# Performance work log

Hardware: AMD Instinct MI355X
Metric: run time of the kernel (lower is better)

The kernel has to match this reference:

```python
import jax, jax.numpy as jnp
import numpy as np
from jax import lax

EPS = 1e-8

def setup_inputs() -> dict:
    key = jax.random.key(0)
    k1, k2, k3, k4 = jax.random.split(key, 4)
    b, ic, oc, ks, sd, h, w = 16, 512, 512, 3, 512, 64, 64
    x = jax.random.normal(k1, (b, ic, h, w), dtype=jnp.float32)
    style = jax.random.normal(k2, (b, sd), dtype=jnp.float32)
    # kaiming_normal_(fan_in, linear): std = 1/sqrt(ic*ks*ks)
    weight = jax.random.normal(k3, (oc, ic, ks, ks), dtype=jnp.float32) / np.sqrt(ic * ks * ks)
    bias = jnp.zeros((oc,), dtype=jnp.float32)
    # nn.Linear default init ~ U(-1/sqrt(sd), 1/sqrt(sd)); normal approx is fine for a baseline
    mod_w = jax.random.normal(k4, (ic, sd), dtype=jnp.float32) / np.sqrt(sd)
    mod_b = jnp.ones((ic,), dtype=jnp.float32)  # bias initialized to 1.0 in the module
    return {"x": x, "style": style, "weight": weight, "bias": bias, "mod_w": mod_w, "mod_b": mod_b}

def reference(x, style, weight, bias, mod_w, mod_b):
    b, ic, h, w = x.shape
    oc, _, ks, _ = weight.shape
    # style modulation: [b, ic]
    s = style @ mod_w.T + mod_b
    # per-sample modulated weights: [b, oc, ic, k, k]
    wmod = weight[None] * s[:, None, :, None, None]
    # demodulation
    demod = lax.rsqrt(jnp.sum(wmod * wmod, axis=(2, 3, 4)) + EPS)  # [b, oc]
    wmod = wmod * demod[:, :, None, None, None]
    pad = ks // 2
    # grouped conv with groups=b == per-sample conv: vmap over batch
    def conv1(xi, wi):  # xi: [ic,h,w], wi: [oc,ic,k,k]
        return lax.conv_general_dilated(
            xi[None], wi, window_strides=(1, 1),
            padding=[(pad, pad), (pad, pad)],
            dimension_numbers=("NCHW", "OIHW", "NCHW"))[0]
    out = jax.vmap(conv1)(x, wmod)  # [b, oc, h, w]
    return out + bias[None, :, None, None]
```

## Files before the change

kernel.cpp:

```cpp
#include <hip/hip_runtime.h>
#include <hip/hip_bf16.h>


typedef __bf16 bf16x8 __attribute__((ext_vector_type(8)));
typedef float  f32x4  __attribute__((ext_vector_type(4)));

#define IC   512
#define OC   512
#define HW   4096
#define KTOT 4608

typedef __attribute__((address_space(3))) unsigned lds_u32;
typedef const __attribute__((address_space(1))) unsigned glb_u32;
#define GLL16(gsrc, ldst) \
    __builtin_amdgcn_global_load_lds((glb_u32*)(gsrc), (lds_u32*)(ldst), 16, 0, 0)
#define VMW(N)  asm volatile("s_waitcnt vmcnt(" #N ")" ::: "memory")
#define BAR()   asm volatile("s_barrier" ::: "memory")
#define SCHED0() __builtin_amdgcn_sched_barrier(0)

__global__ __launch_bounds__(256) void style_mod_kernel(
    const float* __restrict__ style, const float* __restrict__ mod_w,
    const float* __restrict__ mod_b, float* __restrict__ s_out)
{
    int pair = blockIdx.x * 4 + (threadIdx.x >> 6);
    int lane = threadIdx.x & 63;
    int b = pair >> 9;
    int i = pair & 511;
    const float4* sv = (const float4*)(style + b * 512);
    const float4* wv = (const float4*)(mod_w + i * 512);
    float4 a0 = sv[lane * 2], a1 = sv[lane * 2 + 1];
    float4 w0 = wv[lane * 2], w1 = wv[lane * 2 + 1];
    float sum = a0.x*w0.x + a0.y*w0.y + a0.z*w0.z + a0.w*w0.w
              + a1.x*w1.x + a1.y*w1.y + a1.z*w1.z + a1.w*w1.w;
    #pragma unroll
    for (int off = 32; off; off >>= 1) sum += __shfl_xor(sum, off);
    if (lane == 0) s_out[pair] = sum + mod_b[i];
}

__global__ __launch_bounds__(256) void wmod_kernel(
    const float* __restrict__ weight,
    const float* __restrict__ s_in,
    __hip_bfloat16* __restrict__ wmod)
{
    int b  = blockIdx.x >> 9;
    int oc = blockIdx.x & 511;
    __shared__ float s_sh[512];
    __shared__ float red[256];
    int t = threadIdx.x;
    s_sh[t]       = s_in[b * 512 + t];
    s_sh[t + 256] = s_in[b * 512 + t + 256];
    __syncthreads();
    const float* wrow = weight + (size_t)oc * KTOT;
    float partial = 0.f;
    for (int e = t; e < KTOT; e += 256) {
        float v = wrow[e] * s_sh[e / 9];
        partial += v * v;
    }
    red[t] = partial;
    __syncthreads();
    #pragma unroll
    for (int off = 128; off; off >>= 1) {
        if (t < off) red[t] += red[t + off];
        __syncthreads();
    }
    float demod = rsqrtf(red[0] + 1e-8f);
    __hip_bfloat16* dst = wmod + (size_t)blockIdx.x * KTOT;
    for (int ep = t; ep < KTOT; ep += 256) {
        int tap = ep >> 9, ic = ep & 511;
        dst[ep] = __float2bfloat16(wrow[ic * 9 + tap] * s_sh[ic] * demod);
    }
}

__global__ void zero_row_kernel(__hip_bfloat16* xT) {
    ((unsigned*)(xT + ((size_t)blockIdx.x * 4097 + 4096) * 512))[threadIdx.x] = 0u;
}

__global__ __launch_bounds__(256) void xpose_kernel(
    const float* __restrict__ x, __hip_bfloat16* __restrict__ xT)
{
    __shared__ __align__(16) float tile[64][68];
    int b = blockIdx.z, ic0 = blockIdx.y * 64, p0 = blockIdx.x * 64;
    int t = threadIdx.x;
    const float* xb = x + ((size_t)b * 512 + ic0) * 4096 + p0;
    int rr = t >> 4, cc = (t & 15) * 4;
    #pragma unroll
    for (int i = 0; i < 4; ++i) {
        float4 v = *(const float4*)(xb + (size_t)(rr + i * 16) * 4096 + cc);
        *(float4*)&tile[rr + i * 16][cc] = v;
    }
    __syncthreads();
    int pr = t >> 2, io = (t & 3) * 16;
    __hip_bfloat16 obuf[16];
    #pragma unroll
    for (int j = 0; j < 16; ++j) obuf[j] = __float2bfloat16(tile[io + j][pr]);
    __hip_bfloat16* dst = xT + ((size_t)b * 4097 + p0 + pr) * 512 + ic0 + io;
    *(uint4*)dst       = *(uint4*)&obuf[0];
    *(uint4*)(dst + 8) = *(uint4*)&obuf[8];
}

__global__ __launch_bounds__(512, 2) void conv_kernel(
    const __hip_bfloat16* __restrict__ xT,
    const __hip_bfloat16* __restrict__ wmod,
    const float* __restrict__ bias,
    float* __restrict__ out)
{
    __shared__ __align__(16) __hip_bfloat16 Ash[4][256 * 32];
    __shared__ __align__(16) __hip_bfloat16 Bsh[4][256 * 32];

    const int t    = threadIdx.x;
    const int lane = t & 63;
    const int wid  = t >> 6;
    const int wm   = wid >> 2;
    const int wn   = wid & 3;
    const int lr   = lane & 15;
    const int lq   = lane >> 4;

    int bid = blockIdx.x;
    int xcd = bid & 7, idx = bid >> 3;
    int oc1 = idx & 1;
    int nt  = (idx >> 1) & 15;
    int bb  = (idx >> 5) & 1;
    int b   = xcd * 2 + bb;
    int oc0 = oc1 * 256, n0 = nt * 256;

    const __hip_bfloat16* wb = wmod + (size_t)(b * 512 + oc0) * KTOT;
    const __hip_bfloat16* xb = xT + (size_t)b * 4097 * 512;

    const int qoff = (((t & 3) ^ ((t >> 3) & 3)) * 8);
    const int srow = t >> 2;
    const int p0g  = n0 + srow;
    const int y0p  = p0g >> 6, x0p = p0g & 63;

    const __hip_bfloat16* pA0 = wb + (size_t)srow * KTOT + qoff;
    const __hip_bfloat16* pA1 = pA0 + (size_t)128 * KTOT;

    const int swq = (lq ^ ((lr >> 1) & 3)) * 8;
    const int arb = (wm * 128 + lr) * 32 + swq;
    const int brb = (wn * 64  + lr) * 32 + swq;

    f32x4 acc[8][4] = {};

    auto bptrs = [&](int tap, const __hip_bfloat16*& P0, const __hip_bfloat16*& P1) {
        int dy = tap / 3 - 1, dx = tap % 3 - 1;
        int sy = y0p + dy, sx = x0p + dx;
        int pix0 = ((((unsigned)sy)  < 64u) & (((unsigned)sx) < 64u)) ? ((sy  << 6) + sx) : 4096;
        int sy1 = sy + 2;
        int pix1 = ((((unsigned)sy1) < 64u) & (((unsigned)sx) < 64u)) ? ((sy1 << 6) + sx) : 4096;
        P0 = xb + (size_t)pix0 * 512 + qoff;
        P1 = xb + (size_t)pix1 * 512 + qoff;
    };

#define STAGE_A(SB, OFF) { \
    GLL16(pA0 + (OFF), &Ash[SB][t * 8]); \
    GLL16(pA1 + (OFF), &Ash[SB][(t + 512) * 8]); }
#define STAGE_B(SB, Q0, Q1, OFF) { \
    GLL16((Q0) + (OFF), &Bsh[SB][t * 8]); \
    GLL16((Q1) + (OFF), &Bsh[SB][(t + 512) * 8]); }

#define MFMA_HALF(MB) { \
    __builtin_amdgcn_s_setprio(1); \
    _Pragma("unroll") for (int mi = 0; mi < 4; ++mi) \
        _Pragma("unroll") for (int ni = 0; ni < 4; ++ni) \
            acc[(MB) + mi][ni] = __builtin_amdgcn_mfma_f32_16x16x32_bf16( \
                af[mi], bfr[ni], acc[(MB) + mi][ni], 0, 0, 0); \
    __builtin_amdgcn_s_setprio(0); }

    const __hip_bfloat16 *pB0, *pB1, *nB0, *nB1;
    bptrs(0, pB0, pB1);

    STAGE_A(0, 0);  STAGE_B(0, pB0, pB1, 0);
    STAGE_A(1, 32); STAGE_B(1, pB0, pB1, 32);
    STAGE_A(2, 64); STAGE_B(2, pB0, pB1, 64);
    VMW(8);
    BAR();

    for (int tap = 0; tap < 8; ++tap) {
        bptrs(tap + 1, nB0, nB1);
        #pragma unroll
        for (int ch = 0; ch < 16; ++ch) {
            const int cb = ch & 3, sb = (ch + 3) & 3;
            bf16x8 af[4], bfr[4];
            #pragma unroll
            for (int mi = 0; mi < 4; ++mi)
                af[mi] = *(const bf16x8*)(&Ash[cb][arb + mi * 512]);
            #pragma unroll
            for (int ni = 0; ni < 4; ++ni)
                bfr[ni] = *(const bf16x8*)(&Bsh[cb][brb + ni * 512]);
            STAGE_A(sb, (ch + 3) * 32);
            BAR(); SCHED0();
            MFMA_HALF(0);
            BAR();
            #pragma unroll
            for (int mi = 0; mi < 4; ++mi)
                af[mi] = *(const bf16x8*)(&Ash[cb][arb + (4 + mi) * 512]);
            if (ch < 13) { STAGE_B(sb, pB0, pB1, (ch + 3) * 32); }
            else         { STAGE_B(sb, nB0, nB1, (ch - 13) * 32); }
            BAR(); SCHED0();
            MFMA_HALF(4);
            VMW(8);
            BAR();
        }
        pA0 += 512; pA1 += 512;
        pB0 = nB0; pB1 = nB1;
    }
    #pragma unroll
    for (int ch = 0; ch < 16; ++ch) {
        const int cb = ch & 3, sb = (ch + 3) & 3;
        bf16x8 af[4], bfr[4];
        #pragma unroll
        for (int mi = 0; mi < 4; ++mi)
            af[mi] = *(const bf16x8*)(&Ash[cb][arb + mi * 512]);
        #pragma unroll
        for (int ni = 0; ni < 4; ++ni)
            bfr[ni] = *(const bf16x8*)(&Bsh[cb][brb + ni * 512]);
        if (ch <= 12) STAGE_A(sb, (ch + 3) * 32);
        BAR(); SCHED0();
        MFMA_HALF(0);
        BAR();
        #pragma unroll
        for (int mi = 0; mi < 4; ++mi)
            af[mi] = *(const bf16x8*)(&Ash[cb][arb + (4 + mi) * 512]);
        if (ch <= 12) STAGE_B(sb, pB0, pB1, (ch + 3) * 32);
        BAR(); SCHED0();
        MFMA_HALF(4);
        if      (ch < 13)  { VMW(8); BAR(); }
        else if (ch == 13) { VMW(4); BAR(); }
        else if (ch == 14) { VMW(0); BAR(); }
    }
#undef STAGE_A
#undef STAGE_B
#undef MFMA_HALF

    #pragma unroll
    for (int mi = 0; mi < 8; ++mi) {
        int oc = oc0 + wm * 128 + mi * 16 + lq * 4;
        #pragma unroll
        for (int ni = 0; ni < 4; ++ni) {
            int n = n0 + wn * 64 + ni * 16 + lr;
            #pragma unroll
            for (int v = 0; v < 4; ++v) {
                float r = acc[mi][ni][v] + bias[oc + v];
                out[((size_t)(b * OC + oc + v)) * HW + n] = r;
            }
        }
    }
}

extern "C" void kernel_launch(void* const* d_in, const int* in_sizes, int n_in,
                              void* d_out, int out_size, void* d_ws, size_t ws_size,
                              hipStream_t stream) {
    const float* x      = (const float*)d_in[0];
    const float* style  = (const float*)d_in[1];
    const float* weight = (const float*)d_in[2];
    const float* bias   = (const float*)d_in[3];
    const float* mod_w  = (const float*)d_in[4];
    const float* mod_b  = (const float*)d_in[5];
    float* out = (float*)d_out;

    float* s_ws = (float*)d_ws;
    __hip_bfloat16* wmod = (__hip_bfloat16*)((char*)d_ws + 32768);
    __hip_bfloat16* xT   = (__hip_bfloat16*)((char*)d_ws + 32768 + (size_t)16 * 512 * KTOT * 2);

    style_mod_kernel<<<2048, 256, 0, stream>>>(style, mod_w, mod_b, s_ws);
    wmod_kernel<<<16 * 512, 256, 0, stream>>>(weight, s_ws, wmod);
    zero_row_kernel<<<16, 256, 0, stream>>>(xT);
    dim3 tgrid(64, 8, 16);
    xpose_kernel<<<tgrid, 256, 0, stream>>>(x, xT);
    conv_kernel<<<512, 512, 0, stream>>>(xT, wmod, bias, out);
}
```

Baseline: 374.3 us.

## Restructure weight modulation per output channel, sharing weight row across batch

```diff
diff --git a/kernel.cpp b/kernel.cpp
--- a/kernel.cpp
+++ b/kernel.cpp
@@ -42,32 +42,41 @@
     const float* __restrict__ s_in,
     __hip_bfloat16* __restrict__ wmod)
 {
-    int b  = blockIdx.x >> 9;
-    int oc = blockIdx.x & 511;
-    __shared__ float s_sh[512];
-    __shared__ float red[256];
+    int oc = blockIdx.x;
+    __shared__ float w_sh[4608];
+    __shared__ float s_sh[8192];
+    __shared__ float q_sh[512];
+    __shared__ float demod_sh[16];
     int t = threadIdx.x;
-    s_sh[t]       = s_in[b * 512 + t];
-    s_sh[t + 256] = s_in[b * 512 + t + 256];
-    __syncthreads();
     const float* wrow = weight + (size_t)oc * KTOT;
-    float partial = 0.f;
-    for (int e = t; e < KTOT; e += 256) {
-        float v = wrow[e] * s_sh[e / 9];
-        partial += v * v;
-    }
-    red[t] = partial;
-    __syncthreads();
-    #pragma unroll
-    for (int off = 128; off; off >>= 1) {
-        if (t < off) red[t] += red[t + off];
-        __syncthreads();
-    }
-    float demod = rsqrtf(red[0] + 1e-8f);
-    __hip_bfloat16* dst = wmod + (size_t)blockIdx.x * KTOT;
-    for (int ep = t; ep < KTOT; ep += 256) {
-        int tap = ep >> 9, ic = ep & 511;
-        dst[ep] = __float2bfloat16(wrow[ic * 9 + tap] * s_sh[ic] * demod);
+    for (int e = t; e < 4608; e += 256) w_sh[e] = wrow[e];
+    for (int e = t; e < 8192; e += 256) s_sh[e] = s_in[e];
+    __syncthreads();
+    for (int ic = t; ic < 512; ic += 256) {
+        float q = 0.f;
+        #pragma unroll
+        for (int tap = 0; tap < 9; ++tap) { float w = w_sh[ic * 9 + tap]; q += w * w; }
+        q_sh[ic] = q;
+    }
+    __syncthreads();
+    int bb = t >> 4, li = t & 15;
+    float part = 0.f;
+    for (int ic = li; ic < 512; ic += 16) {
+        float sv = s_sh[bb * 512 + ic];
+        part += q_sh[ic] * sv * sv;
+    }
+    #pragma unroll
+    for (int off = 8; off; off >>= 1) part += __shfl_xor(part, off, 16);
+    if (li == 0) demod_sh[bb] = rsqrtf(part + 1e-8f);
+    __syncthreads();
+    for (int b2 = 0; b2 < 16; ++b2) {
+        float dm = demod_sh[b2];
+        const float* srow = s_sh + b2 * 512;
+        __hip_bfloat16* dst = wmod + ((size_t)b2 * 512 + oc) * KTOT;
+        for (int ep = t; ep < 4608; ep += 256) {
+            int tap = ep >> 9, ic = ep & 511;
+            dst[ep] = __float2bfloat16(w_sh[ic * 9 + tap] * srow[ic] * dm);
+        }
     }
 }
 
@@ -262,7 +271,7 @@
     __hip_bfloat16* xT   = (__hip_bfloat16*)((char*)d_ws + 32768 + (size_t)16 * 512 * KTOT * 2);
 
     style_mod_kernel<<<2048, 256, 0, stream>>>(style, mod_w, mod_b, s_ws);
-    wmod_kernel<<<16 * 512, 256, 0, stream>>>(weight, s_ws, wmod);
+    wmod_kernel<<<512, 256, 0, stream>>>(weight, s_ws, wmod);
     zero_row_kernel<<<16, 256, 0, stream>>>(xT);
     dim3 tgrid(64, 8, 16);
     xpose_kernel<<<tgrid, 256, 0, stream>>>(x, xT);
```

Measured after the change: 339.0 us. 1.1x faster.
